# Performance work log

Hardware: AMD Instinct MI355X
Metric: run time of the kernel (lower is better)

Reference implementation:

```python
import jax, jax.numpy as jnp
import numpy as np

B, T, D, V, MEM = 2, 512, 512, 256, 256


def _gru(x, h0, wih, whh, bih, bhh):
    # x: [B,T,D], h0: [B,D]; torch GRU gate order: r, z, n
    def step(h, xt):
        gi = xt @ wih.T + bih            # [B,3D]
        gh = h @ whh.T + bhh             # [B,3D]
        i_r, i_z, i_n = jnp.split(gi, 3, axis=-1)
        h_r, h_z, h_n = jnp.split(gh, 3, axis=-1)
        r = jax.nn.sigmoid(i_r + h_r)
        z = jax.nn.sigmoid(i_z + h_z)
        n = jnp.tanh(i_n + r * h_n)
        h_new = (1.0 - z) * n + z * h
        return h_new, h_new
    hT, ys = jax.lax.scan(step, h0, jnp.swapaxes(x, 0, 1))
    return jnp.swapaxes(ys, 0, 1), hT


def _layernorm(x, g, b, eps=1e-5):
    m = jnp.mean(x, axis=-1, keepdims=True)
    v = jnp.mean((x - m) ** 2, axis=-1, keepdims=True)
    return (x - m) / jnp.sqrt(v + eps) * g + b


def setup_inputs() -> dict:
    key = jax.random.key(0)
    ks = jax.random.split(key, 24)
    s = 1.0 / np.sqrt(D)
    inp = {
        'x': jax.random.randint(ks[0], (B, T), 0, V, dtype=jnp.int32),
        'h_f': jnp.zeros((1, B, D), jnp.float32),
        'h_s': jnp.zeros((1, B, D), jnp.float32),
        'soma_w': jax.random.normal(ks[1], (V, D), jnp.float32),
        'fast_wih': jax.random.normal(ks[2], (3 * D, D)) * s,
        'fast_whh': jax.random.normal(ks[3], (3 * D, D)) * s,
        'fast_bih': jax.random.normal(ks[4], (3 * D,)) * s,
        'fast_bhh': jax.random.normal(ks[5], (3 * D,)) * s,
        'slow_wih': jax.random.normal(ks[6], (3 * D, D)) * s,
        'slow_whh': jax.random.normal(ks[7], (3 * D, D)) * s,
        'slow_bih': jax.random.normal(ks[8], (3 * D,)) * s,
        'slow_bhh': jax.random.normal(ks[9], (3 * D,)) * s,
        'qkv_w': jax.random.normal(ks[10], (3 * D, D)) * s,
        'qkv_b': jax.random.normal(ks[11], (3 * D,)) * s,
        'gate_w': jax.random.normal(ks[12], (D, D)) * s,
        'gate_b': jax.random.normal(ks[13], (D,)) * s,
        'gate_g': jnp.ones((D,), jnp.float32),
        'gate_bb': jnp.zeros((D,), jnp.float32),
        'mem_bank': jax.random.normal(ks[14], (MEM, D)) * 0.1,
        'hip_qw': jax.random.normal(ks[15], (D, D)) * s,
        'hip_qb': jax.random.normal(ks[16], (D,)) * s,
        'axon_w': jax.random.normal(ks[17], (D, 4 * D)) * (0.5 * s),
        'axon_b': jax.random.normal(ks[18], (D,)) * s,
        'norm_g': jnp.ones((D,), jnp.float32),
        'norm_b': jnp.zeros((D,), jnp.float32),
    }
    return inp


def reference(x, h_f, h_s, soma_w, fast_wih, fast_whh, fast_bih, fast_bhh,
              slow_wih, slow_whh, slow_bih, slow_bhh, qkv_w, qkv_b,
              gate_w, gate_b, gate_g, gate_bb, mem_bank, hip_qw, hip_qb,
              axon_w, axon_b, norm_g, norm_b):
    d = soma_w.shape[1]
    s_in = soma_w[x]  # mod[0] == 1.0
    p_f, hf1 = _gru(s_in, h_f[0], fast_wih, fast_whh, fast_bih, fast_bhh)
    p_s, hs1 = _gru(p_f, h_s[0], slow_wih, slow_whh, slow_bih, slow_bhh)
    # LinearIntentMemory: naive cumulative outer-product linear attention
    qkv = p_s @ qkv_w.T + qkv_b
    q, k, v = jnp.split(qkv, 3, axis=-1)
    q = jax.nn.elu(q) + 1.0
    k = jax.nn.elu(k) + 1.0
    kv_cum = jnp.cumsum(jnp.einsum('bti,btj->btij', k, v), axis=1)  # [B,T,D,D]
    num = jnp.einsum('bti,btij->btj', q, kv_cum)
    den = jnp.einsum('bti,bti->bt', q, jnp.cumsum(k, axis=1))[..., None] + 1e-6
    l_mem = num / den
    # intent gate: Linear -> LayerNorm -> Tanh
    intent = jnp.tanh(_layernorm(p_s @ gate_w.T + gate_b, gate_g, gate_bb))
    # hippocampus: softmax attention over memory bank
    qh = p_s @ hip_qw.T + hip_qb
    attn = qh @ mem_bank.T / jnp.sqrt(jnp.float32(d))
    episodes = jax.nn.softmax(attn, axis=-1) @ mem_bank
    combined = jnp.concatenate([p_f, intent, l_mem, episodes], axis=-1)
    thought = _layernorm(jnp.tanh(combined @ axon_w.T + axon_b), norm_g, norm_b)
    sw = soma_w / jnp.maximum(jnp.linalg.norm(soma_w, axis=-1, keepdims=True), 1e-12)
    logits = (thought @ sw.T) * 16.0
    return (logits, thought, hf1[None], hs1[None])
```

## Files before the change

kernel.cpp:

```cpp
#include <hip/hip_runtime.h>
#include <cstddef>

#define F_ELUQK 1
#define F_CAUSAL 2
#define F_DIV 4
#define F_NN 8
#define F_SCALE 16
#define F_ROWSUM 32
#define FLAG_STRIDE 4
#define L_WGS 64
#define UNITS 8

enum : int {
  OFF_QH = 0,
  OFF_COMB = 524288,
  OFF_PS = OFF_COMB + 2097152,
  OFF_QKV = OFF_PS + 524288,
  OFF_SCORES = OFF_QKV + 1572864,
  OFF_DEN = OFF_SCORES + 524288,
  OFF_TMP = OFF_DEN + 1024,
  OFF_ATTN = OFF_TMP + 524288,
  OFF_SWN = OFF_ATTN + 262144,
  OFF_RING = OFF_SWN + 256,
  OFF_HSB = OFF_RING + 8192,
  OFF_FLAGS = OFF_HSB + 4096,
  OFF_GIC = OFF_FLAGS + 512
};

#define BAR() __asm__ __volatile__("s_waitcnt lgkmcnt(0)\n\ts_barrier" ::: "memory")

__global__ __launch_bounds__(256) void gemm(
    const float* __restrict__ A, int lda, const float* __restrict__ B, int ldb,
    float* __restrict__ C, int ldc, int coff, int K,
    const float* __restrict__ bias, const float* __restrict__ den,
    const float* __restrict__ cscale, float* __restrict__ rsum,
    float scale, int flags, int bBatch,
    float* __restrict__ Cz, int kzoff) {
  __shared__ float As[16 * 65];
  __shared__ float Bs[16 * 65];
  int tid = threadIdx.x;
  int n0 = blockIdx.x * 64, m0 = blockIdx.y * 64;
  if (blockIdx.z) { A += kzoff; B += kzoff; C = Cz; bias = nullptr; }
  int rowoff = (m0 >> 9) * bBatch;
  int tx = tid & 15, ty = tid >> 4;

  if ((flags & F_CAUSAL) && n0 > ((m0 & 511) + 63)) {
    #pragma unroll
    for (int i = 0; i < 4; ++i)
      #pragma unroll
      for (int j = 0; j < 4; ++j)
        C[(size_t)(m0 + ty * 4 + i) * ldc + coff + n0 + tx * 4 + j] = 0.f;
    return;
  }

  float acc[4][4] = {};
  for (int k0 = 0; k0 < K; k0 += 16) {
    {
      int rr = tid >> 2, c4 = (tid & 3) << 2;
      const float* ap = A + (size_t)(m0 + rr) * lda + (k0 + c4);
      float4 av = *(const float4*)ap;
      As[(c4 + 0) * 65 + rr] = av.x;
      As[(c4 + 1) * 65 + rr] = av.y;
      As[(c4 + 2) * 65 + rr] = av.z;
      As[(c4 + 3) * 65 + rr] = av.w;
    }
    if (!(flags & F_NN)) {
      int rr = tid >> 2, c4 = (tid & 3) << 2;
      const float* bp = B + (size_t)(n0 + rr + rowoff) * ldb + (k0 + c4);
      float4 bv = *(const float4*)bp;
      Bs[(c4 + 0) * 65 + rr] = bv.x; Bs[(c4 + 1) * 65 + rr] = bv.y;
      Bs[(c4 + 2) * 65 + rr] = bv.z; Bs[(c4 + 3) * 65 + rr] = bv.w;
    } else {
      int kk = tid >> 4, n4 = (tid & 15) << 2;
      const float* bp = B + (size_t)(k0 + kk + rowoff) * ldb + (n0 + n4);
      float4 bv = *(const float4*)bp;
      Bs[kk * 65 + n4 + 0] = bv.x; Bs[kk * 65 + n4 + 1] = bv.y;
      Bs[kk * 65 + n4 + 2] = bv.z; Bs[kk * 65 + n4 + 3] = bv.w;
    }
    __syncthreads();
    #pragma unroll
    for (int k = 0; k < 16; ++k) {
      float av[4], bv[4];
      #pragma unroll
      for (int i = 0; i < 4; ++i) av[i] = As[k * 65 + ty * 4 + i];
      #pragma unroll
      for (int j = 0; j < 4; ++j) bv[j] = Bs[k * 65 + tx * 4 + j];
      #pragma unroll
      for (int i = 0; i < 4; ++i)
        #pragma unroll
        for (int j = 0; j < 4; ++j)
          acc[i][j] = fmaf(av[i], bv[j], acc[i][j]);
    }
    __syncthreads();
  }
  float rs[4] = {0.f, 0.f, 0.f, 0.f};
  #pragma unroll
  for (int i = 0; i < 4; ++i) {
    int m = m0 + ty * 4 + i;
    float dv = (flags & F_DIV) ? (1.0f / (den[m] + 1e-6f)) : 1.0f;
    #pragma unroll
    for (int j = 0; j < 4; ++j) {
      int n = n0 + tx * 4 + j;
      float v = acc[i][j];
      if (bias) v += bias[n];
      if (flags & F_ELUQK) { if (n < 1024) v = (v > 0.f) ? (v + 1.f) : __expf(v); }
      if (flags & F_CAUSAL) { if (n > (m & 511)) v = 0.f; }
      if (flags & F_SCALE) v *= scale;
      if (cscale) v *= cscale[coff + n];
      if (flags & F_DIV) v *= dv;
      C[(size_t)m * ldc + coff + n] = v;
      if (flags & F_ROWSUM) rs[i] += v;
    }
  }
  if (flags & F_ROWSUM) {
    #pragma unroll
    for (int i = 0; i < 4; ++i) {
      float s = rs[i];
      s += __shfl_xor(s, 1); s += __shfl_xor(s, 2);
      s += __shfl_xor(s, 4); s += __shfl_xor(s, 8);
      if (tx == 0) atomicAdd(rsum + (m0 + ty * 4 + i), s);
    }
  }
}

__global__ __launch_bounds__(256) void gemm3(
    const float* __restrict__ A,
    const float* __restrict__ qkvw, const float* __restrict__ qkvb,
    const float* __restrict__ gatew, const float* __restrict__ gateb,
    const float* __restrict__ hipw, const float* __restrict__ hipb,
    float* __restrict__ QKV, float* __restrict__ TMP, float* __restrict__ QH) {
  __shared__ float As[16 * 65];
  __shared__ float Bs[16 * 65];
  int tid = threadIdx.x;
  int n0 = blockIdx.x * 64, m0 = blockIdx.y * 64;
  const float* B; const float* bias; float* C; int ldc, base;
  if (n0 < 1536) { B = qkvw; bias = qkvb; C = QKV; ldc = 1536; base = 0; }
  else if (n0 < 2048) { B = gatew; bias = gateb; C = TMP; ldc = 512; base = 1536; }
  else { B = hipw; bias = hipb; C = QH; ldc = 512; base = 2048; }
  int tx = tid & 15, ty = tid >> 4;
  float acc[4][4] = {};
  for (int k0 = 0; k0 < 512; k0 += 16) {
    {
      int rr = tid >> 2, c4 = (tid & 3) << 2;
      const float* ap = A + (size_t)(m0 + rr) * 512 + (k0 + c4);
      float4 av = *(const float4*)ap;
      As[(c4 + 0) * 65 + rr] = av.x; As[(c4 + 1) * 65 + rr] = av.y;
      As[(c4 + 2) * 65 + rr] = av.z; As[(c4 + 3) * 65 + rr] = av.w;
    }
    {
      int rr = tid >> 2, c4 = (tid & 3) << 2;
      const float* bp = B + (size_t)(n0 - base + rr) * 512 + (k0 + c4);
      float4 bv = *(const float4*)bp;
      Bs[(c4 + 0) * 65 + rr] = bv.x; Bs[(c4 + 1) * 65 + rr] = bv.y;
      Bs[(c4 + 2) * 65 + rr] = bv.z; Bs[(c4 + 3) * 65 + rr] = bv.w;
    }
    __syncthreads();
    #pragma unroll
    for (int k = 0; k < 16; ++k) {
      float av[4], bv[4];
      #pragma unroll
      for (int i = 0; i < 4; ++i) av[i] = As[k * 65 + ty * 4 + i];
      #pragma unroll
      for (int j = 0; j < 4; ++j) bv[j] = Bs[k * 65 + tx * 4 + j];
      #pragma unroll
      for (int i = 0; i < 4; ++i)
        #pragma unroll
        for (int j = 0; j < 4; ++j)
          acc[i][j] = fmaf(av[i], bv[j], acc[i][j]);
    }
    __syncthreads();
  }
  #pragma unroll
  for (int i = 0; i < 4; ++i) {
    int m = m0 + ty * 4 + i;
    #pragma unroll
    for (int j = 0; j < 4; ++j) {
      int n = n0 + tx * 4 + j;
      float v = acc[i][j] + bias[n - base];
      if (n < 1024) v = (v > 0.f) ? (v + 1.f) : __expf(v);
      C[(size_t)m * ldc + (n - base)] = v;
    }
  }
}

__device__ __forceinline__ void post_flag(unsigned* flags, int w, unsigned v) {
  __hip_atomic_store(flags + (size_t)w * FLAG_STRIDE, v, __ATOMIC_RELAXED,
                     __HIP_MEMORY_SCOPE_AGENT);
}
__device__ __forceinline__ void poll64(const unsigned* flags, unsigned tgt, int lane) {
  const unsigned* p = flags + (size_t)lane * FLAG_STRIDE;
  while (__hip_atomic_load(p, __ATOMIC_RELAXED, __HIP_MEMORY_SCOPE_AGENT) < tgt)
    __builtin_amdgcn_s_sleep(1);
}
__device__ __forceinline__ void tagload16(const unsigned long long* __restrict__ src,
                                          unsigned expect, int lane,
                                          float* __restrict__ dstLds) {
  unsigned long long v[16];
  for (;;) {
    #pragma unroll
    for (int k = 0; k < 16; ++k)
      v[k] = __hip_atomic_load(src + k * 64 + lane, __ATOMIC_RELAXED,
                               __HIP_MEMORY_SCOPE_AGENT);
    unsigned bad = 0;
    #pragma unroll
    for (int k = 0; k < 16; ++k) bad |= ((unsigned)(v[k] >> 32)) ^ expect;
    if (__all(bad == 0)) break;
    __builtin_amdgcn_s_sleep(1);
  }
  #pragma unroll
  for (int k = 0; k < 16; ++k)
    dstLds[k * 64 + lane] = __uint_as_float((unsigned)v[k]);
}
__device__ __forceinline__ void stage_pull(const unsigned long long* __restrict__ src,
                                           const unsigned* __restrict__ flags,
                                           unsigned tgt, int lane,
                                           float* __restrict__ dstLds) {
  unsigned long long v[16];
  #pragma unroll
  for (int k = 0; k < 16; ++k)
    v[k] = __hip_atomic_load(src + k * 64 + lane, __ATOMIC_RELAXED,
                             __HIP_MEMORY_SCOPE_AGENT);
  unsigned bad = 0;
  #pragma unroll
  for (int k = 0; k < 16; ++k) bad |= ((unsigned)(v[k] >> 32)) ^ tgt;
  if (!__all(bad == 0)) {
    poll64(flags, tgt, lane);
    for (;;) {
      #pragma unroll
      for (int k = 0; k < 16; ++k)
        v[k] = __hip_atomic_load(src + k * 64 + lane, __ATOMIC_RELAXED,
                                 __HIP_MEMORY_SCOPE_AGENT);
      bad = 0;
      #pragma unroll
      for (int k = 0; k < 16; ++k) bad |= ((unsigned)(v[k] >> 32)) ^ tgt;
      if (__all(bad == 0)) break;
      __builtin_amdgcn_s_sleep(1);
    }
  }
  #pragma unroll
  for (int k = 0; k < 16; ++k)
    dstLds[k * 64 + lane] = __uint_as_float((unsigned)v[k]);
}

__global__ __launch_bounds__(256, 1) void gru2_kernel(
    const float* __restrict__ soma, const int* __restrict__ x,
    const float* __restrict__ fwih, const float* __restrict__ fbih,
    const float* __restrict__ fwhh, const float* __restrict__ fbhh,
    const float* __restrict__ h0f,
    const float* __restrict__ swih, const float* __restrict__ sbih,
    const float* __restrict__ swhh, const float* __restrict__ sbhh,
    const float* __restrict__ h0s,
    float* __restrict__ pf_out,
    float* __restrict__ ps_out,
    float* __restrict__ hfT, float* __restrict__ hsT,
    unsigned long long* __restrict__ ringq,
    unsigned long long* __restrict__ hsq,
    unsigned* __restrict__ flagsA, unsigned* __restrict__ flagsB,
    float* __restrict__ gi,
    unsigned* __restrict__ gic) {
  __shared__ __attribute__((aligned(16))) float hl[1024];
  __shared__ __attribute__((aligned(16))) float inb[2048];
  __shared__ float P[48];
  __shared__ float Q[48];
  __shared__ float bl[24];
  __shared__ float bi[24];
  __shared__ float As2[16 * 65];
  __shared__ float Bs2[16 * 65];
  __shared__ int xs[64];
  int tid = threadIdx.x, wg = blockIdx.x;

  if (wg >= 2 * L_WGS) {
    int gw = wg - 2 * L_WGS;
    int tx = tid & 15, ty = tid >> 4;
    for (int g = gw; g < 384; g += 64) {
      int c = g / 24, ct = g - c * 24;
      int cbase = c * 32, n0 = ct * 64;
      if (tid < 64) xs[tid] = x[cbase + (tid & 31) + ((tid >> 5) << 9)];
      __syncthreads();
      float acc[4][4] = {};
      for (int k0 = 0; k0 < 512; k0 += 16) {
        {
          int rr = tid >> 2, c4 = (tid & 3) << 2;
          const float* ap = soma + (size_t)xs[rr] * 512 + (k0 + c4);
          float4 av = *(const float4*)ap;
          As2[(c4 + 0) * 65 + rr] = av.x; As2[(c4 + 1) * 65 + rr] = av.y;
          As2[(c4 + 2) * 65 + rr] = av.z; As2[(c4 + 3) * 65 + rr] = av.w;
          const float* bp = fwih + (size_t)(n0 + rr) * 512 + (k0 + c4);
          float4 bv = *(const float4*)bp;
          Bs2[(c4 + 0) * 65 + rr] = bv.x; Bs2[(c4 + 1) * 65 + rr] = bv.y;
          Bs2[(c4 + 2) * 65 + rr] = bv.z; Bs2[(c4 + 3) * 65 + rr] = bv.w;
        }
        __syncthreads();
        #pragma unroll
        for (int k = 0; k < 16; ++k) {
          float av[4], bv[4];
          #pragma unroll
          for (int i = 0; i < 4; ++i) av[i] = As2[k * 65 + ty * 4 + i];
          #pragma unroll
          for (int j = 0; j < 4; ++j) bv[j] = Bs2[k * 65 + tx * 4 + j];
          #pragma unroll
          for (int i = 0; i < 4; ++i)
            #pragma unroll
            for (int j = 0; j < 4; ++j)
              acc[i][j] = fmaf(av[i], bv[j], acc[i][j]);
        }
        __syncthreads();
      }
      #pragma unroll
      for (int i = 0; i < 4; ++i) {
        int rr = ty * 4 + i;
        int m = cbase + (rr & 31) + ((rr >> 5) << 9);
        #pragma unroll
        for (int j = 0; j < 4; ++j)
          gi[(size_t)m * 1536 + n0 + tx * 4 + j] = acc[i][j];
      }
      __threadfence();
      __syncthreads();
      if (tid == 0)
        __hip_atomic_fetch_add(gic + c, 1u, __ATOMIC_RELEASE,
                               __HIP_MEMORY_SCOPE_AGENT);
    }
    return;
  }

  bool L1 = wg < L_WGS;
  int j0 = (wg & (L_WGS - 1)) * UNITS;
  int part = tid & 7, r = tid >> 3;
  int g = r >> 3, u = r & 7;
  int wave = tid >> 6, lane = tid & 63;
  const float* whh = L1 ? fwhh : swhh;
  const float* bhh = L1 ? fbhh : sbhh;
  const float* bihp = L1 ? fbih : sbih;

  float4 wh[16], wi[16];
  if (r < 24) {
    const float* wp = whh + (size_t)(g * 512 + j0 + u) * 512 + part * 4;
    #pragma unroll
    for (int i = 0; i < 16; ++i) wh[i] = *(const float4*)(wp + i * 32);
    if (!L1) {
      const float* wp2 = swih + (size_t)(g * 512 + j0 + u) * 512 + part * 4;
      #pragma unroll
      for (int i = 0; i < 16; ++i) wi[i] = *(const float4*)(wp2 + i * 32);
    }
  }
  if (tid < 24) {
    bl[tid] = bhh[(tid >> 3) * 512 + j0 + (tid & 7)];
    bi[tid] = bihp[(tid >> 3) * 512 + j0 + (tid & 7)];
  }
  __syncthreads();

  if (!L1 && wave == 3) {
    stage_pull(ringq, flagsA, 1u, lane, inb);
  }
  BAR();

  const float4* h4 = (const float4*)hl;

  if (L1) {
    for (int t = 0; t < 512; ++t) {
      float gi_r = 0.f, gi_z = 0.f, gi_n = 0.f;
      if (wave == 3) {
        if ((t & 31) == 0) {
          const unsigned* gc = gic + (t >> 5);
          while (__hip_atomic_load(gc, __ATOMIC_ACQUIRE,
                                   __HIP_MEMORY_SCOPE_AGENT) < 24u)
            __builtin_amdgcn_s_sleep(1);
        }
        if (lane < 16) {
          const float* gp = gi + (size_t)((lane >> 3) * 512 + t) * 1536
                              + j0 + (lane & 7);
          gi_r = gp[0]; gi_z = gp[512]; gi_n = gp[1024];
        }
        if (t == 0) {
          #pragma unroll
          for (int k = 0; k < 16; ++k) hl[k * 64 + lane] = h0f[k * 64 + lane];
        } else {
          poll64(flagsA, (unsigned)t, lane);
          tagload16(ringq + (size_t)((t - 1) & 3) * 1024, (unsigned)t, lane, hl);
        }
      }
      BAR();
      if (wave != 3) {
        float a0 = 0.f, a1 = 0.f;
        #pragma unroll
        for (int i = 0; i < 16; ++i) {
          float4 w = wh[i];
          float4 x0 = h4[i * 8 + part];
          float4 x1 = h4[128 + i * 8 + part];
          a0 += w.x * x0.x + w.y * x0.y + w.z * x0.z + w.w * x0.w;
          a1 += w.x * x1.x + w.y * x1.y + w.z * x1.z + w.w * x1.w;
        }
        a0 += __shfl_xor(a0, 1); a0 += __shfl_xor(a0, 2); a0 += __shfl_xor(a0, 4);
        a1 += __shfl_xor(a1, 1); a1 += __shfl_xor(a1, 2); a1 += __shfl_xor(a1, 4);
        if (part == 0 && r < 24) { P[r] = a0; P[24 + r] = a1; }
      } else {
        if (t >= 4) poll64(flagsB, (unsigned)(t - 3), lane);
      }
      BAR();
      if (wave == 3 && lane < 16) {
        int b = lane >> 3, u2 = lane & 7, j = j0 + u2;
        float i_r = gi_r + bi[u2];
        float i_z = gi_z + bi[8 + u2];
        float i_n = gi_n + bi[16 + u2];
        float gh_r = P[b * 24 + u2] + bl[u2];
        float gh_z = P[b * 24 + 8 + u2] + bl[8 + u2];
        float gh_n = P[b * 24 + 16 + u2] + bl[16 + u2];
        float hold = hl[b * 512 + j];
        float rg = 1.0f / (1.0f + __expf(-(i_r + gh_r)));
        float zg = 1.0f / (1.0f + __expf(-(i_z + gh_z)));
        float ng = tanhf(i_n + rg * gh_n);
        float hnew = (1.0f - zg) * ng + zg * hold;
        unsigned long long pv =
            ((unsigned long long)(unsigned)(t + 1) << 32) |
            (unsigned long long)__float_as_uint(hnew);
        __hip_atomic_store(ringq + (size_t)(t & 3) * 1024 + b * 512 + j, pv,
                           __ATOMIC_RELAXED, __HIP_MEMORY_SCOPE_AGENT);
        if (lane == 0) post_flag(flagsA, wg, (unsigned)(t + 1));
        pf_out[(size_t)(b * 512 + t) * 2048 + j] = hnew;
        if (t == 511) hfT[b * 512 + j] = hnew;
      }
    }
  } else {
    for (int t2 = 0; t2 < 512; ++t2) {
      float c0 = 0.f, c1 = 0.f;
      if (wave == 3) {
        if (t2 == 0) {
          #pragma unroll
          for (int k = 0; k < 16; ++k) hl[k * 64 + lane] = h0s[k * 64 + lane];
        }
        if (t2 + 1 < 512) {
          stage_pull(ringq + (size_t)((t2 + 1) & 3) * 1024, flagsA,
                     (unsigned)(t2 + 2), lane, inb + ((t2 + 1) & 1) * 1024);
          __builtin_amdgcn_sched_barrier(0);
        }
        if (t2 > 0) {
          stage_pull(hsq + (size_t)((t2 - 1) & 1) * 1024, flagsB,
                     (unsigned)t2, lane, hl);
        }
      } else {
        const float4* f4v = (const float4*)(inb + (t2 & 1) * 1024);
        #pragma unroll
        for (int i = 0; i < 16; ++i) {
          float4 v = wi[i];
          float4 y0 = f4v[i * 8 + part];
          float4 y1 = f4v[128 + i * 8 + part];
          c0 += v.x * y0.x + v.y * y0.y + v.z * y0.z + v.w * y0.w;
          c1 += v.x * y1.x + v.y * y1.y + v.z * y1.z + v.w * y1.w;
        }
      }
      BAR();
      if (wave != 3) {
        float a0 = 0.f, a1 = 0.f;
        #pragma unroll
        for (int i = 0; i < 16; ++i) {
          float4 w = wh[i];
          float4 x0 = h4[i * 8 + part];
          float4 x1 = h4[128 + i * 8 + part];
          a0 += w.x * x0.x + w.y * x0.y + w.z * x0.z + w.w * x0.w;
          a1 += w.x * x1.x + w.y * x1.y + w.z * x1.z + w.w * x1.w;
        }
        a0 += __shfl_xor(a0, 1); a0 += __shfl_xor(a0, 2); a0 += __shfl_xor(a0, 4);
        a1 += __shfl_xor(a1, 1); a1 += __shfl_xor(a1, 2); a1 += __shfl_xor(a1, 4);
        c0 += __shfl_xor(c0, 1); c0 += __shfl_xor(c0, 2); c0 += __shfl_xor(c0, 4);
        c1 += __shfl_xor(c1, 1); c1 += __shfl_xor(c1, 2); c1 += __shfl_xor(c1, 4);
        if (part == 0 && r < 24) { P[r] = a0; P[24 + r] = a1; Q[r] = c0; Q[24 + r] = c1; }
      }
      BAR();
      if (wave == 3 && lane < 16) {
        int b = lane >> 3, u2 = lane & 7, j = j0 + u2;
        float i_r = Q[b * 24 + u2] + bi[u2];
        float i_z = Q[b * 24 + 8 + u2] + bi[8 + u2];
        float i_n = Q[b * 24 + 16 + u2] + bi[16 + u2];
        float gh_r = P[b * 24 + u2] + bl[u2];
        float gh_z = P[b * 24 + 8 + u2] + bl[8 + u2];
        float gh_n = P[b * 24 + 16 + u2] + bl[16 + u2];
        float hold = hl[b * 512 + j];
        float rg = 1.0f / (1.0f + __expf(-(i_r + gh_r)));
        float zg = 1.0f / (1.0f + __expf(-(i_z + gh_z)));
        float ng = tanhf(i_n + rg * gh_n);
        float hnew = (1.0f - zg) * ng + zg * hold;
        unsigned long long pv =
            ((unsigned long long)(unsigned)(t2 + 1) << 32) |
            (unsigned long long)__float_as_uint(hnew);
        __hip_atomic_store(hsq + (size_t)(t2 & 1) * 1024 + b * 512 + j, pv,
                           __ATOMIC_RELAXED, __HIP_MEMORY_SCOPE_AGENT);
        if (lane == 0) post_flag(flagsB, wg - L_WGS, (unsigned)(t2 + 1));
        ps_out[(size_t)(b * 512 + t2) * 512 + j] = hnew;
        if (t2 == 511) hsT[b * 512 + j] = hnew;
      }
    }
  }
}

__global__ __launch_bounds__(256) void softmax_kernel(float* __restrict__ a) {
  int m = blockIdx.x, tid = threadIdx.x;
  float v = a[(size_t)m * 256 + tid];
  float mx = v;
  #pragma unroll
  for (int off = 32; off > 0; off >>= 1) mx = fmaxf(mx, __shfl_down(mx, off));
  __shared__ float r4[4];
  __shared__ float s4[4];
  if ((tid & 63) == 0) r4[tid >> 6] = mx;
  __syncthreads();
  mx = fmaxf(fmaxf(r4[0], r4[1]), fmaxf(r4[2], r4[3]));
  float e = __expf(v - mx);
  float s = e;
  #pragma unroll
  for (int off = 32; off > 0; off >>= 1) s += __shfl_down(s, off);
  if ((tid & 63) == 0) s4[tid >> 6] = s;
  __syncthreads();
  s = s4[0] + s4[1] + s4[2] + s4[3];
  a[(size_t)m * 256 + tid] = e / s;
}

__global__ __launch_bounds__(256) void ln_kernel(
    const float* __restrict__ src, const float* __restrict__ src2,
    float* __restrict__ dst, int ldd, int dcoff,
    const float* __restrict__ gv, const float* __restrict__ bv, int tanhFirst) {
  int m = blockIdx.x, tid = threadIdx.x;
  float x0 = src[(size_t)m * 512 + tid];
  float x1 = src[(size_t)m * 512 + 256 + tid];
  if (src2) { x0 += src2[(size_t)m * 512 + tid]; x1 += src2[(size_t)m * 512 + 256 + tid]; }
  if (tanhFirst) { x0 = tanhf(x0); x1 = tanhf(x1); }
  float s = x0 + x1, ss = x0 * x0 + x1 * x1;
  #pragma unroll
  for (int off = 32; off > 0; off >>= 1) { s += __shfl_down(s, off); ss += __shfl_down(ss, off); }
  __shared__ float rs[4], rss[4];
  if ((tid & 63) == 0) { rs[tid >> 6] = s; rss[tid >> 6] = ss; }
  __syncthreads();
  float st = rs[0] + rs[1] + rs[2] + rs[3];
  float sst = rss[0] + rss[1] + rss[2] + rss[3];
  float mean = st * (1.0f / 512.0f);
  float var = sst * (1.0f / 512.0f) - mean * mean;
  float inv = rsqrtf(var + 1e-5f);
  float y0 = (x0 - mean) * inv * gv[tid] + bv[tid];
  float y1 = (x1 - mean) * inv * gv[256 + tid] + bv[256 + tid];
  if (!tanhFirst) { y0 = tanhf(y0); y1 = tanhf(y1); }
  dst[(size_t)m * ldd + dcoff + tid] = y0;
  dst[(size_t)m * ldd + dcoff + 256 + tid] = y1;
}

__global__ __launch_bounds__(256) void swinv_kernel(const float* __restrict__ soma,
                                                    float* __restrict__ swn) {
  int r = blockIdx.x, tid = threadIdx.x;
  float x0 = soma[(size_t)r * 512 + tid];
  float x1 = soma[(size_t)r * 512 + 256 + tid];
  float ss = x0 * x0 + x1 * x1;
  #pragma unroll
  for (int off = 32; off > 0; off >>= 1) ss += __shfl_down(ss, off);
  __shared__ float r4[4];
  if ((tid & 63) == 0) r4[tid >> 6] = ss;
  __syncthreads();
  if (tid == 0) {
    float norm = fmaxf(sqrtf(r4[0] + r4[1] + r4[2] + r4[3]), 1e-12f);
    swn[r] = 16.0f / norm;
  }
}

extern "C" void kernel_launch(void* const* d_in, const int* in_sizes, int n_in,
                              void* d_out, int out_size, void* d_ws, size_t ws_size,
                              hipStream_t stream) {
  (void)in_sizes; (void)n_in; (void)out_size; (void)ws_size;
  float* W = (float*)d_ws;
  float* outf = (float*)d_out;
  const int* x = (const int*)d_in[0];
  const float* soma = (const float*)d_in[3];

  hipMemsetAsync((char*)d_ws + (size_t)OFF_RING * 4, 0, 51264, stream);
  hipMemsetAsync((char*)d_ws + (size_t)OFF_DEN * 4, 0, 4096, stream);

  gru2_kernel<<<3 * L_WGS, 256, 0, stream>>>(soma, x,
      (const float*)d_in[4], (const float*)d_in[6],
      (const float*)d_in[5], (const float*)d_in[7], (const float*)d_in[1],
      (const float*)d_in[8], (const float*)d_in[10],
      (const float*)d_in[9], (const float*)d_in[11], (const float*)d_in[2],
      W + OFF_COMB, W + OFF_PS, outf + 786432, outf + 787456,
      (unsigned long long*)(W + OFF_RING), (unsigned long long*)(W + OFF_HSB),
      (unsigned*)(W + OFF_FLAGS),
      (unsigned*)(W + OFF_FLAGS) + L_WGS * FLAG_STRIDE,
      W + OFF_QKV, (unsigned*)(W + OFF_GIC));

  gemm3<<<dim3(40, 16), 256, 0, stream>>>(W + OFF_PS,
      (const float*)d_in[12], (const float*)d_in[13],
      (const float*)d_in[14], (const float*)d_in[15],
      (const float*)d_in[19], (const float*)d_in[20],
      W + OFF_QKV, W + OFF_TMP, W + OFF_QH);

  gemm<<<dim3(8, 16), 256, 0, stream>>>(W + OFF_QKV, 1536, W + OFF_QKV + 512, 1536,
      W + OFF_SCORES, 512, 0, 512, nullptr, nullptr, nullptr, W + OFF_DEN,
      1.f, F_CAUSAL | F_ROWSUM, 512, nullptr, 0);

  gemm<<<dim3(8, 16), 256, 0, stream>>>(W + OFF_SCORES, 512, W + OFF_QKV + 1024, 1536,
      W + OFF_COMB, 2048, 1024, 512, nullptr, W + OFF_DEN, nullptr, nullptr,
      1.f, F_NN | F_DIV, 512, nullptr, 0);

  ln_kernel<<<1024, 256, 0, stream>>>(W + OFF_TMP, nullptr, W + OFF_COMB, 2048, 512,
      (const float*)d_in[16], (const float*)d_in[17], 0);

  gemm<<<dim3(4, 16), 256, 0, stream>>>(W + OFF_QH, 512, (const float*)d_in[18], 512,
      W + OFF_ATTN, 256, 0, 512, nullptr, nullptr, nullptr, nullptr,
      0.04419417382415922f, F_SCALE, 0, nullptr, 0);
  softmax_kernel<<<1024, 256, 0, stream>>>(W + OFF_ATTN);
  gemm<<<dim3(8, 16), 256, 0, stream>>>(W + OFF_ATTN, 256, (const float*)d_in[18], 512,
      W + OFF_COMB, 2048, 1536, 256, nullptr, nullptr, nullptr, nullptr,
      1.f, F_NN, 0, nullptr, 0);

  gemm<<<dim3(8, 16, 2), 256, 0, stream>>>(W + OFF_COMB, 2048, (const float*)d_in[21], 2048,
      W + OFF_TMP, 512, 0, 1024, (const float*)d_in[22], nullptr, nullptr, nullptr,
      1.f, 0, 0, W + OFF_QH, 1024);

  ln_kernel<<<1024, 256, 0, stream>>>(W + OFF_TMP, W + OFF_QH, outf + 262144, 512, 0,
      (const float*)d_in[23], (const float*)d_in[24], 1);

  swinv_kernel<<<256, 256, 0, stream>>>(soma, W + OFF_SWN);
  gemm<<<dim3(4, 16), 256, 0, stream>>>(outf + 262144, 512, soma, 512,
      outf, 256, 0, 512, nullptr, nullptr, W + OFF_SWN, nullptr,
      1.f, 0, 0, nullptr, 0);
}
```

Baseline: 1.905 ms.

## Split input-gate GEMM into separate kernel and batch flag polling

The embedding-times-W_ih GEMM that previously ran in extra workgroups of the persistent GRU kernel, gated by per-chunk counters, now runs as its own kernel before the GRU launch. This removes the per-32-step counter waits and the extra co-resident workgroups. The GRU loop also drops the r<24 guard on partial-sum writes and issues its gi loads ahead of a scheduling barrier. The poll loop now takes four staggered flag loads per iteration with longer sleeps. The cost is that the GEMM can no longer overlap the start of the recurrence, and the polling change may add wake-up latency on the critical recurrent path.

```diff
diff --git a/kernel.cpp b/kernel.cpp
--- a/kernel.cpp
+++ b/kernel.cpp
@@ -23,8 +23,7 @@
   OFF_SWN = OFF_ATTN + 262144,
   OFF_RING = OFF_SWN + 256,
   OFF_HSB = OFF_RING + 8192,
-  OFF_FLAGS = OFF_HSB + 4096,
-  OFF_GIC = OFF_FLAGS + 512
+  OFF_FLAGS = OFF_HSB + 4096
 };
 
 #define BAR() __asm__ __volatile__("s_waitcnt lgkmcnt(0)\n\ts_barrier" ::: "memory")
@@ -183,14 +182,78 @@
   }
 }
 
+__global__ __launch_bounds__(256) void gi_kernel(
+    const float* __restrict__ soma, const int* __restrict__ x,
+    const float* __restrict__ fwih, float* __restrict__ gi) {
+  __shared__ float As2[16 * 65];
+  __shared__ float Bs2[16 * 65];
+  __shared__ int xs[64];
+  int tid = threadIdx.x;
+  int g = blockIdx.x;
+  int c = g / 24, ct = g - c * 24;
+  int cbase = c * 32, n0 = ct * 64;
+  int tx = tid & 15, ty = tid >> 4;
+  if (tid < 64) xs[tid] = x[cbase + (tid & 31) + ((tid >> 5) << 9)];
+  __syncthreads();
+  float acc[4][4] = {};
+  for (int k0 = 0; k0 < 512; k0 += 16) {
+    {
+      int rr = tid >> 2, c4 = (tid & 3) << 2;
+      const float* ap = soma + (size_t)xs[rr] * 512 + (k0 + c4);
+      float4 av = *(const float4*)ap;
+      As2[(c4 + 0) * 65 + rr] = av.x; As2[(c4 + 1) * 65 + rr] = av.y;
+      As2[(c4 + 2) * 65 + rr] = av.z; As2[(c4 + 3) * 65 + rr] = av.w;
+      const float* bp = fwih + (size_t)(n0 + rr) * 512 + (k0 + c4);
+      float4 bv = *(const float4*)bp;
+      Bs2[(c4 + 0) * 65 + rr] = bv.x; Bs2[(c4 + 1) * 65 + rr] = bv.y;
+      Bs2[(c4 + 2) * 65 + rr] = bv.z; Bs2[(c4 + 3) * 65 + rr] = bv.w;
+    }
+    __syncthreads();
+    #pragma unroll
+    for (int k = 0; k < 16; ++k) {
+      float av[4], bv[4];
+      #pragma unroll
+      for (int i = 0; i < 4; ++i) av[i] = As2[k * 65 + ty * 4 + i];
+      #pragma unroll
+      for (int j = 0; j < 4; ++j) bv[j] = Bs2[k * 65 + tx * 4 + j];
+      #pragma unroll
+      for (int i = 0; i < 4; ++i)
+        #pragma unroll
+        for (int j = 0; j < 4; ++j)
+          acc[i][j] = fmaf(av[i], bv[j], acc[i][j]);
+    }
+    __syncthreads();
+  }
+  #pragma unroll
+  for (int i = 0; i < 4; ++i) {
+    int rr = ty * 4 + i;
+    int m = cbase + (rr & 31) + ((rr >> 5) << 9);
+    #pragma unroll
+    for (int j = 0; j < 4; ++j)
+      gi[(size_t)m * 1536 + n0 + tx * 4 + j] = acc[i][j];
+  }
+}
+
 __device__ __forceinline__ void post_flag(unsigned* flags, int w, unsigned v) {
   __hip_atomic_store(flags + (size_t)w * FLAG_STRIDE, v, __ATOMIC_RELAXED,
                      __HIP_MEMORY_SCOPE_AGENT);
 }
 __device__ __forceinline__ void poll64(const unsigned* flags, unsigned tgt, int lane) {
   const unsigned* p = flags + (size_t)lane * FLAG_STRIDE;
-  while (__hip_atomic_load(p, __ATOMIC_RELAXED, __HIP_MEMORY_SCOPE_AGENT) < tgt)
-    __builtin_amdgcn_s_sleep(1);
+  for (;;) {
+    unsigned f0 = __hip_atomic_load(p, __ATOMIC_RELAXED, __HIP_MEMORY_SCOPE_AGENT);
+    __builtin_amdgcn_s_sleep(4);
+    unsigned f1 = __hip_atomic_load(p, __ATOMIC_RELAXED, __HIP_MEMORY_SCOPE_AGENT);
+    __builtin_amdgcn_s_sleep(4);
+    unsigned f2 = __hip_atomic_load(p, __ATOMIC_RELAXED, __HIP_MEMORY_SCOPE_AGENT);
+    __builtin_amdgcn_s_sleep(4);
+    unsigned f3 = __hip_atomic_load(p, __ATOMIC_RELAXED, __HIP_MEMORY_SCOPE_AGENT);
+    if (__all(f0 >= tgt)) break;
+    if (__all(f1 >= tgt)) break;
+    if (__all(f2 >= tgt)) break;
+    if (__all(f3 >= tgt)) break;
+    __builtin_amdgcn_s_sleep(2);
+  }
 }
 __device__ __forceinline__ void tagload16(const unsigned long long* __restrict__ src,
                                           unsigned expect, int lane,
@@ -243,10 +306,9 @@
 }
 
 __global__ __launch_bounds__(256, 1) void gru2_kernel(
-    const float* __restrict__ soma, const int* __restrict__ x,
-    const float* __restrict__ fwih, const float* __restrict__ fbih,
-    const float* __restrict__ fwhh, const float* __restrict__ fbhh,
-    const float* __restrict__ h0f,
+    const float* __restrict__ gi,
+    const float* __restrict__ fwhh, const float* __restrict__ fbih,
+    const float* __restrict__ fbhh, const float* __restrict__ h0f,
     const float* __restrict__ swih, const float* __restrict__ sbih,
     const float* __restrict__ swhh, const float* __restrict__ sbhh,
     const float* __restrict__ h0s,
@@ -255,74 +317,14 @@
     float* __restrict__ hfT, float* __restrict__ hsT,
     unsigned long long* __restrict__ ringq,
     unsigned long long* __restrict__ hsq,
-    unsigned* __restrict__ flagsA, unsigned* __restrict__ flagsB,
-    float* __restrict__ gi,
-    unsigned* __restrict__ gic) {
+    unsigned* __restrict__ flagsA, unsigned* __restrict__ flagsB) {
   __shared__ __attribute__((aligned(16))) float hl[1024];
   __shared__ __attribute__((aligned(16))) float inb[2048];
   __shared__ float P[48];
   __shared__ float Q[48];
   __shared__ float bl[24];
   __shared__ float bi[24];
-  __shared__ float As2[16 * 65];
-  __shared__ float Bs2[16 * 65];
-  __shared__ int xs[64];
   int tid = threadIdx.x, wg = blockIdx.x;
-
-  if (wg >= 2 * L_WGS) {
-    int gw = wg - 2 * L_WGS;
-    int tx = tid & 15, ty = tid >> 4;
-    for (int g = gw; g < 384; g += 64) {
-      int c = g / 24, ct = g - c * 24;
-      int cbase = c * 32, n0 = ct * 64;
-      if (tid < 64) xs[tid] = x[cbase + (tid & 31) + ((tid >> 5) << 9)];
-      __syncthreads();
-      float acc[4][4] = {};
-      for (int k0 = 0; k0 < 512; k0 += 16) {
-        {
-          int rr = tid >> 2, c4 = (tid & 3) << 2;
-          const float* ap = soma + (size_t)xs[rr] * 512 + (k0 + c4);
-          float4 av = *(const float4*)ap;
-          As2[(c4 + 0) * 65 + rr] = av.x; As2[(c4 + 1) * 65 + rr] = av.y;
-          As2[(c4 + 2) * 65 + rr] = av.z; As2[(c4 + 3) * 65 + rr] = av.w;
-          const float* bp = fwih + (size_t)(n0 + rr) * 512 + (k0 + c4);
-          float4 bv = *(const float4*)bp;
-          Bs2[(c4 + 0) * 65 + rr] = bv.x; Bs2[(c4 + 1) * 65 + rr] = bv.y;
-          Bs2[(c4 + 2) * 65 + rr] = bv.z; Bs2[(c4 + 3) * 65 + rr] = bv.w;
-        }
-        __syncthreads();
-        #pragma unroll
-        for (int k = 0; k < 16; ++k) {
-          float av[4], bv[4];
-          #pragma unroll
-          for (int i = 0; i < 4; ++i) av[i] = As2[k * 65 + ty * 4 + i];
-          #pragma unroll
-          for (int j = 0; j < 4; ++j) bv[j] = Bs2[k * 65 + tx * 4 + j];
-          #pragma unroll
-          for (int i = 0; i < 4; ++i)
-            #pragma unroll
-            for (int j = 0; j < 4; ++j)
-              acc[i][j] = fmaf(av[i], bv[j], acc[i][j]);
-        }
-        __syncthreads();
-      }
-      #pragma unroll
-      for (int i = 0; i < 4; ++i) {
-        int rr = ty * 4 + i;
-        int m = cbase + (rr & 31) + ((rr >> 5) << 9);
-        #pragma unroll
-        for (int j = 0; j < 4; ++j)
-          gi[(size_t)m * 1536 + n0 + tx * 4 + j] = acc[i][j];
-      }
-      __threadfence();
-      __syncthreads();
-      if (tid == 0)
-        __hip_atomic_fetch_add(gic + c, 1u, __ATOMIC_RELEASE,
-                               __HIP_MEMORY_SCOPE_AGENT);
-    }
-    return;
-  }
-
   bool L1 = wg < L_WGS;
   int j0 = (wg & (L_WGS - 1)) * UNITS;
   int part = tid & 7, r = tid >> 3;
@@ -357,20 +359,15 @@
   const float4* h4 = (const float4*)hl;
 
   if (L1) {
+    float gA = 0.f, gB = 0.f, gC = 0.f;
     for (int t = 0; t < 512; ++t) {
-      float gi_r = 0.f, gi_z = 0.f, gi_n = 0.f;
       if (wave == 3) {
-        if ((t & 31) == 0) {
-          const unsigned* gc = gic + (t >> 5);
-          while (__hip_atomic_load(gc, __ATOMIC_ACQUIRE,
-                                   __HIP_MEMORY_SCOPE_AGENT) < 24u)
-            __builtin_amdgcn_s_sleep(1);
-        }
         if (lane < 16) {
           const float* gp = gi + (size_t)((lane >> 3) * 512 + t) * 1536
                               + j0 + (lane & 7);
-          gi_r = gp[0]; gi_z = gp[512]; gi_n = gp[1024];
-        }
+          gA = gp[0]; gB = gp[512]; gC = gp[1024];
+        }
+        __builtin_amdgcn_sched_barrier(0);
         if (t == 0) {
           #pragma unroll
           for (int k = 0; k < 16; ++k) hl[k * 64 + lane] = h0f[k * 64 + lane];
@@ -392,16 +389,16 @@
         }
         a0 += __shfl_xor(a0, 1); a0 += __shfl_xor(a0, 2); a0 += __shfl_xor(a0, 4);
         a1 += __shfl_xor(a1, 1); a1 += __shfl_xor(a1, 2); a1 += __shfl_xor(a1, 4);
-        if (part == 0 && r < 24) { P[r] = a0; P[24 + r] = a1; }
+        if (part == 0) { P[r] = a0; P[24 + r] = a1; }
       } else {
         if (t >= 4) poll64(flagsB, (unsigned)(t - 3), lane);
       }
       BAR();
       if (wave == 3 && lane < 16) {
         int b = lane >> 3, u2 = lane & 7, j = j0 + u2;
-        float i_r = gi_r + bi[u2];
-        float i_z = gi_z + bi[8 + u2];
-        float i_n = gi_n + bi[16 + u2];
+        float i_r = gA + bi[u2];
+        float i_z = gB + bi[8 + u2];
+        float i_n = gC + bi[16 + u2];
         float gh_r = P[b * 24 + u2] + bl[u2];
         float gh_z = P[b * 24 + 8 + u2] + bl[8 + u2];
         float gh_n = P[b * 24 + 16 + u2] + bl[16 + u2];
@@ -463,7 +460,7 @@
         a1 += __shfl_xor(a1, 1); a1 += __shfl_xor(a1, 2); a1 += __shfl_xor(a1, 4);
         c0 += __shfl_xor(c0, 1); c0 += __shfl_xor(c0, 2); c0 += __shfl_xor(c0, 4);
         c1 += __shfl_xor(c1, 1); c1 += __shfl_xor(c1, 2); c1 += __shfl_xor(c1, 4);
-        if (part == 0 && r < 24) { P[r] = a0; P[24 + r] = a1; Q[r] = c0; Q[24 + r] = c1; }
+        if (part == 0) { P[r] = a0; P[24 + r] = a1; Q[r] = c0; Q[24 + r] = c1; }
       }
       BAR();
       if (wave == 3 && lane < 16) {
@@ -566,19 +563,21 @@
   const int* x = (const int*)d_in[0];
   const float* soma = (const float*)d_in[3];
 
-  hipMemsetAsync((char*)d_ws + (size_t)OFF_RING * 4, 0, 51264, stream);
+  hipMemsetAsync((char*)d_ws + (size_t)OFF_RING * 4, 0, 51200, stream);
   hipMemsetAsync((char*)d_ws + (size_t)OFF_DEN * 4, 0, 4096, stream);
 
-  gru2_kernel<<<3 * L_WGS, 256, 0, stream>>>(soma, x,
-      (const float*)d_in[4], (const float*)d_in[6],
-      (const float*)d_in[5], (const float*)d_in[7], (const float*)d_in[1],
+  swinv_kernel<<<256, 256, 0, stream>>>(soma, W + OFF_SWN);
+  gi_kernel<<<384, 256, 0, stream>>>(soma, x, (const float*)d_in[4], W + OFF_QKV);
+
+  gru2_kernel<<<2 * L_WGS, 256, 0, stream>>>(W + OFF_QKV,
+      (const float*)d_in[5], (const float*)d_in[6],
+      (const float*)d_in[7], (const float*)d_in[1],
       (const float*)d_in[8], (const float*)d_in[10],
       (const float*)d_in[9], (const float*)d_in[11], (const float*)d_in[2],
       W + OFF_COMB, W + OFF_PS, outf + 786432, outf + 787456,
       (unsigned long long*)(W + OFF_RING), (unsigned long long*)(W + OFF_HSB),
       (unsigned*)(W + OFF_FLAGS),
-      (unsigned*)(W + OFF_FLAGS) + L_WGS * FLAG_STRIDE,
-      W + OFF_QKV, (unsigned*)(W + OFF_GIC));
+      (unsigned*)(W + OFF_FLAGS) + L_WGS * FLAG_STRIDE);
 
   gemm3<<<dim3(40, 16), 256, 0, stream>>>(W + OFF_PS,
       (const float*)d_in[12], (const float*)d_in[13],
@@ -612,7 +611,6 @@
   ln_kernel<<<1024, 256, 0, stream>>>(W + OFF_TMP, W + OFF_QH, outf + 262144, 512, 0,
       (const float*)d_in[23], (const float*)d_in[24], 1);
 
-  swinv_kernel<<<256, 256, 0, stream>>>(soma, W + OFF_SWN);
   gemm<<<dim3(4, 16), 256, 0, stream>>>(outf + 262144, 512, soma, 512,
       outf, 256, 0, 512, nullptr, nullptr, W + OFF_SWN, nullptr,
       1.f, 0, 0, nullptr, 0);
```

New measurement: 1.912 ms. No clear change (+0.4%).
